# Optimization experiments

Hardware: AMD Instinct MI355X
Metric: run time of the kernel (lower is better)

Reference implementation:

```python
import jax, jax.numpy as jnp
import numpy as np

L, N = 200, 256  # event_list_length, num_nodes


def setup_inputs() -> dict:
    key = jax.random.key(0)
    ks = jax.random.split(key, 7)
    time = jax.random.uniform(ks[0], (2,), dtype=jnp.float32)
    event_list = jax.random.normal(ks[1], (L + 1, N, N), dtype=jnp.float32)
    u_begin = jax.random.uniform(ks[2], (N, N, 3), dtype=jnp.float32)
    # xavier-ish scales for params
    a = jax.random.normal(ks[3], (L, N, N, 3), dtype=jnp.float32) * 0.05
    w = jax.random.normal(ks[4], (L, N, 1, N), dtype=jnp.float32) * 0.05
    liner_w = jax.random.normal(ks[5], (N, 3), dtype=jnp.float32) * 0.5
    liner_b = jax.random.normal(ks[6], (N,), dtype=jnp.float32) * 0.1
    return {"time": time, "event_list": event_list, "u_begin": u_begin,
            "a": a, "w": w, "liner_w": liner_w, "liner_b": liner_b,
            "batch_size": 2}


def reference(time, event_list, u_begin, a, w, liner_w, liner_b, batch_size):
    # event_list[:-1]; consumed in pairs (start, start+1) with batch_size == 2
    T = event_list.shape[0] - 1
    S = T // batch_size                      # number of scan steps
    n = event_list.shape[1]
    e2 = event_list[:T].reshape(S, 2, n, n)          # [S,2,N,N]
    a2 = a[:T].reshape(S, 2, n, n, 3)                # [S,2,N,N,3]
    w2 = w[:T, :, 0, :].reshape(S, 2, n, n)          # [S,2,N,N] (squeeze the 1-dim)
    t0, t1 = time[0], time[1]                        # original always uses time[0], time[1]

    def step(u, xs):
        ep, ap, wp = xs                              # [2,N,N], [2,N,N,3], [2,N,N]
        # per-node scalar dot: w[start][node] @ event_begin[k][node]
        dot0 = jnp.einsum('nk,nk->n', wp[0], ep[0])  # [N]
        dot1 = jnp.einsum('nk,nk->n', wp[1], ep[1])
        # math.exp in the original returns a Python float -> constant w.r.t. autograd
        f0 = jax.lax.stop_gradient(jnp.exp(-dot0 * t0))[:, None, None]
        f1 = jax.lax.stop_gradient(jnp.exp(-dot1 * t1))[:, None, None]
        lamda = u + ap[0] * f0 + ap[1] * f1          # [N,N,3]
        temp = jax.nn.softmax(lamda, axis=-1)        # softmax over the 3-dim (dim=1 of [N,3] per node)
        # per-node Linear(3,1): temp[node] @ W_node^T + b_node -> [N,N]
        out = jnp.einsum('nmc,nc->nm', temp, liner_w) + liner_b[:, None]
        # state update was .detach().cpu().numpy() -> stop_gradient
        return jax.lax.stop_gradient(temp), out

    _, outs = jax.lax.scan(step, u_begin, (e2, a2, w2))
    return outs                                      # [S, N, N] == [T/2, N, N]
```

## Files before the change

kernel.cpp:

```cpp
#include <hip/hip_runtime.h>


#define NN 256
#define TT 200
#define SS 100
#define DEPTH 5

__global__ __launch_bounds__(256) void f_kernel(
    const float* __restrict__ timep,
    const float* __restrict__ ev,
    const float* __restrict__ w,
    float* __restrict__ fs)
{
    const int lane = threadIdx.x & 63;
    const int gwave = blockIdx.x * 4 + (threadIdx.x >> 6);
    const int t = gwave >> 8;
    const int n = gwave & 255;

    const size_t rowoff = (size_t)t * (NN * NN) + (size_t)n * NN;
    const float4* wp = (const float4*)(w + rowoff);
    const float4* ep = (const float4*)(ev + rowoff);
    float4 wv = wp[lane];
    float4 evv = ep[lane];
    float d = wv.x * evv.x;
    d = fmaf(wv.y, evv.y, d);
    d = fmaf(wv.z, evv.z, d);
    d = fmaf(wv.w, evv.w, d);
#pragma unroll
    for (int off = 1; off < 64; off <<= 1)
        d += __shfl_xor(d, off, 64);

    if (lane == 0) {
        const float tsel = (t & 1) ? timep[1] : timep[0];
        fs[n * TT + t] = __expf(-d * tsel);
    }
}

__global__ __launch_bounds__(256) void scan_kernel(
    const float* __restrict__ fs_g,
    const float* __restrict__ ub,
    const float* __restrict__ a,
    const float* __restrict__ lw,
    const float* __restrict__ lb,
    float* __restrict__ out)
{
    __shared__ float fs[TT];

    const int n = blockIdx.x;
    const int m = threadIdx.x;

    if (m < TT) fs[m] = fs_g[n * TT + m];
    __syncthreads();

    const size_t base    = (size_t)n * (NN * 3) + (size_t)m * 3;
    const size_t TSTRIDE = (size_t)NN * NN * 3;
    const float* ap = a + base;

    float u0 = ub[base + 0];
    float u1 = ub[base + 1];
    float u2 = ub[base + 2];

    const float w0 = lw[n * 3 + 0];
    const float w1 = lw[n * 3 + 1];
    const float w2 = lw[n * 3 + 2];
    const float bb = lb[n];

    float* op = out + (size_t)n * NN + m;

    float buf[DEPTH][6];
#pragma unroll
    for (int d = 0; d < DEPTH; ++d) {
        const float* app = ap + (size_t)(2 * d) * TSTRIDE;
        buf[d][0] = app[0];
        buf[d][1] = app[1];
        buf[d][2] = app[2];
        buf[d][3] = app[TSTRIDE + 0];
        buf[d][4] = app[TSTRIDE + 1];
        buf[d][5] = app[TSTRIDE + 2];
    }

    for (int s0 = 0; s0 < SS; s0 += DEPTH) {
#pragma unroll
        for (int d = 0; d < DEPTH; ++d) {
            const int s = s0 + d;

            const float f0 = fs[2 * s];
            const float f1 = fs[2 * s + 1];

            float l0 = fmaf(buf[d][0], f0, fmaf(buf[d][3], f1, u0));
            float l1 = fmaf(buf[d][1], f0, fmaf(buf[d][4], f1, u1));
            float l2 = fmaf(buf[d][2], f0, fmaf(buf[d][5], f1, u2));

            const int sp = (s + DEPTH < SS) ? (s + DEPTH) : 0;
            const float* app = ap + (size_t)(2 * sp) * TSTRIDE;
            buf[d][0] = app[0];
            buf[d][1] = app[1];
            buf[d][2] = app[2];
            buf[d][3] = app[TSTRIDE + 0];
            buf[d][4] = app[TSTRIDE + 1];
            buf[d][5] = app[TSTRIDE + 2];

            float mx = fmaxf(l0, fmaxf(l1, l2));
            float e0 = __expf(l0 - mx);
            float e1 = __expf(l1 - mx);
            float e2 = __expf(l2 - mx);
            float inv = __builtin_amdgcn_rcpf(e0 + e1 + e2);
            u0 = e0 * inv;
            u1 = e1 * inv;
            u2 = e2 * inv;
            op[(size_t)s * (NN * NN)] = fmaf(u0, w0, fmaf(u1, w1, fmaf(u2, w2, bb)));
        }
    }
}

extern "C" void kernel_launch(void* const* d_in, const int* in_sizes, int n_in,
                              void* d_out, int out_size, void* d_ws, size_t ws_size,
                              hipStream_t stream) {
    const float* timep = (const float*)d_in[0];
    const float* ev    = (const float*)d_in[1];
    const float* ub    = (const float*)d_in[2];
    const float* a     = (const float*)d_in[3];
    const float* w     = (const float*)d_in[4];
    const float* lw    = (const float*)d_in[5];
    const float* lb    = (const float*)d_in[6];
    float* out = (float*)d_out;
    float* fs  = (float*)d_ws;

    f_kernel<<<(TT * NN) / 4, 256, 0, stream>>>(timep, ev, w, fs);
    scan_kernel<<<NN, 256, 0, stream>>>(fs, ub, a, lw, lb, out);
}
```

Before: 305.7 us.

## Stage scan inputs through double-buffered LDS with async global loads and split rows

```diff
diff --git a/kernel.cpp b/kernel.cpp
--- a/kernel.cpp
+++ b/kernel.cpp
@@ -4,7 +4,15 @@
 #define NN 256
 #define TT 200
 #define SS 100
-#define DEPTH 5
+#define CH 10
+#define SLABS (2*CH)
+#define HALF 128
+#define SEG (HALF*3)
+#define CHUNKF (SLABS*SEG)
+#define NCHUNK (SS/CH)
+
+typedef const __attribute__((address_space(1))) void* gas1;
+typedef __attribute__((address_space(3))) void* las3;
 
 __global__ __launch_bounds__(256) void f_kernel(
     const float* __restrict__ timep,
@@ -12,31 +20,36 @@
     const float* __restrict__ w,
     float* __restrict__ fs)
 {
-    const int lane = threadIdx.x & 63;
+    const int lane  = threadIdx.x & 63;
     const int gwave = blockIdx.x * 4 + (threadIdx.x >> 6);
-    const int t = gwave >> 8;
-    const int n = gwave & 255;
+    const int n  = gwave & 255;
+    const int tp = gwave >> 8;
+    const int ta = 2 * tp;
 
-    const size_t rowoff = (size_t)t * (NN * NN) + (size_t)n * NN;
-    const float4* wp = (const float4*)(w + rowoff);
-    const float4* ep = (const float4*)(ev + rowoff);
-    float4 wv = wp[lane];
-    float4 evv = ep[lane];
-    float d = wv.x * evv.x;
-    d = fmaf(wv.y, evv.y, d);
-    d = fmaf(wv.z, evv.z, d);
-    d = fmaf(wv.w, evv.w, d);
+    const size_t ro_a = (size_t)ta * (NN * NN) + (size_t)n * NN;
+    const size_t ro_b = ro_a + (size_t)(NN * NN);
+    float4 wa = ((const float4*)(w  + ro_a))[lane];
+    float4 ea = ((const float4*)(ev + ro_a))[lane];
+    float4 wb = ((const float4*)(w  + ro_b))[lane];
+    float4 eb = ((const float4*)(ev + ro_b))[lane];
+    float da = wa.x * ea.x;
+    da = fmaf(wa.y, ea.y, da); da = fmaf(wa.z, ea.z, da); da = fmaf(wa.w, ea.w, da);
+    float db = wb.x * eb.x;
+    db = fmaf(wb.y, eb.y, db); db = fmaf(wb.z, eb.z, db); db = fmaf(wb.w, eb.w, db);
 #pragma unroll
-    for (int off = 1; off < 64; off <<= 1)
-        d += __shfl_xor(d, off, 64);
-
+    for (int off = 1; off < 64; off <<= 1) {
+        da += __shfl_xor(da, off, 64);
+        db += __shfl_xor(db, off, 64);
+    }
     if (lane == 0) {
-        const float tsel = (t & 1) ? timep[1] : timep[0];
-        fs[n * TT + t] = __expf(-d * tsel);
+        float2 r;
+        r.x = __expf(-da * timep[0]);
+        r.y = __expf(-db * timep[1]);
+        ((float2*)(fs + (size_t)n * TT))[tp] = r;
     }
 }
 
-__global__ __launch_bounds__(256) void scan_kernel(
+__global__ __launch_bounds__(HALF) void scan_kernel(
     const float* __restrict__ fs_g,
     const float* __restrict__ ub,
     const float* __restrict__ a,
@@ -45,71 +58,70 @@
     float* __restrict__ out)
 {
     __shared__ float fs[TT];
+    __shared__ float buf[2][CHUNKF];
 
-    const int n = blockIdx.x;
-    const int m = threadIdx.x;
+    const int nb   = blockIdx.x >> 1;
+    const int h    = blockIdx.x & 1;
+    const int mm   = threadIdx.x;
+    const int lane = mm & 63;
+    const int wid  = mm >> 6;
 
-    if (m < TT) fs[m] = fs_g[n * TT + m];
+    if (mm < TT) fs[mm] = fs_g[(size_t)nb * TT + mm];
+    if (mm + HALF < TT) fs[mm + HALF] = fs_g[(size_t)nb * TT + mm + HALF];
+
+    const size_t rowbase = (size_t)nb * 768 + (size_t)h * SEG;
+    const size_t TS = (size_t)NN * NN * 3;
+
+    auto fill = [&](int c, int which) {
+#pragma unroll
+        for (int r = 0; r < 15; ++r) {
+            const unsigned base4 = (unsigned)((r * 2 + wid) * 64);
+            const unsigned q  = base4 + (unsigned)lane;
+            const unsigned tl = q / 96;
+            const unsigned o4 = q - tl * 96;
+            const float* g = a + (size_t)(c * SLABS + tl) * TS + rowbase + (size_t)o4 * 4;
+            float* l = &buf[which][(size_t)base4 * 4];
+            __builtin_amdgcn_global_load_lds((gas1)g, (las3)l, 16, 0, 0);
+        }
+    };
+
+    fill(0, 0);
+
+    float u0, u1, u2;
+    {
+        const size_t b = rowbase + (size_t)mm * 3;
+        u0 = ub[b + 0]; u1 = ub[b + 1]; u2 = ub[b + 2];
+    }
+    const float w0 = lw[nb * 3 + 0];
+    const float w1 = lw[nb * 3 + 1];
+    const float w2 = lw[nb * 3 + 2];
+    const float bbias = lb[nb];
+    float* op = out + (size_t)nb * NN + (size_t)h * HALF + mm;
+
     __syncthreads();
 
-    const size_t base    = (size_t)n * (NN * 3) + (size_t)m * 3;
-    const size_t TSTRIDE = (size_t)NN * NN * 3;
-    const float* ap = a + base;
-
-    float u0 = ub[base + 0];
-    float u1 = ub[base + 1];
-    float u2 = ub[base + 2];
-
-    const float w0 = lw[n * 3 + 0];
-    const float w1 = lw[n * 3 + 1];
-    const float w2 = lw[n * 3 + 2];
-    const float bb = lb[n];
-
-    float* op = out + (size_t)n * NN + m;
-
-    float buf[DEPTH][6];
+    for (int c = 0; c < NCHUNK; ++c) {
+        if (c + 1 < NCHUNK) fill(c + 1, (c + 1) & 1);
+        const float* B = buf[c & 1];
 #pragma unroll
-    for (int d = 0; d < DEPTH; ++d) {
-        const float* app = ap + (size_t)(2 * d) * TSTRIDE;
-        buf[d][0] = app[0];
-        buf[d][1] = app[1];
-        buf[d][2] = app[2];
-        buf[d][3] = app[TSTRIDE + 0];
-        buf[d][4] = app[TSTRIDE + 1];
-        buf[d][5] = app[TSTRIDE + 2];
-    }
-
-    for (int s0 = 0; s0 < SS; s0 += DEPTH) {
-#pragma unroll
-        for (int d = 0; d < DEPTH; ++d) {
-            const int s = s0 + d;
-
+        for (int k = 0; k < CH; ++k) {
+            const int s = c * CH + k;
+            const float* s0 = B + (size_t)(2 * k) * SEG + (size_t)mm * 3;
+            const float* s1 = s0 + SEG;
             const float f0 = fs[2 * s];
             const float f1 = fs[2 * s + 1];
-
-            float l0 = fmaf(buf[d][0], f0, fmaf(buf[d][3], f1, u0));
-            float l1 = fmaf(buf[d][1], f0, fmaf(buf[d][4], f1, u1));
-            float l2 = fmaf(buf[d][2], f0, fmaf(buf[d][5], f1, u2));
-
-            const int sp = (s + DEPTH < SS) ? (s + DEPTH) : 0;
-            const float* app = ap + (size_t)(2 * sp) * TSTRIDE;
-            buf[d][0] = app[0];
-            buf[d][1] = app[1];
-            buf[d][2] = app[2];
-            buf[d][3] = app[TSTRIDE + 0];
-            buf[d][4] = app[TSTRIDE + 1];
-            buf[d][5] = app[TSTRIDE + 2];
-
+            float l0 = fmaf(s0[0], f0, fmaf(s1[0], f1, u0));
+            float l1 = fmaf(s0[1], f0, fmaf(s1[1], f1, u1));
+            float l2 = fmaf(s0[2], f0, fmaf(s1[2], f1, u2));
             float mx = fmaxf(l0, fmaxf(l1, l2));
             float e0 = __expf(l0 - mx);
             float e1 = __expf(l1 - mx);
             float e2 = __expf(l2 - mx);
             float inv = __builtin_amdgcn_rcpf(e0 + e1 + e2);
-            u0 = e0 * inv;
-            u1 = e1 * inv;
-            u2 = e2 * inv;
-            op[(size_t)s * (NN * NN)] = fmaf(u0, w0, fmaf(u1, w1, fmaf(u2, w2, bb)));
+            u0 = e0 * inv; u1 = e1 * inv; u2 = e2 * inv;
+            op[(size_t)s * (NN * NN)] = fmaf(u0, w0, fmaf(u1, w1, fmaf(u2, w2, bbias)));
         }
+        __syncthreads();
     }
 }
 
@@ -126,6 +138,6 @@
     float* out = (float*)d_out;
     float* fs  = (float*)d_ws;
 
-    f_kernel<<<(TT * NN) / 4, 256, 0, stream>>>(timep, ev, w, fs);
-    scan_kernel<<<NN, 256, 0, stream>>>(fs, ub, a, lw, lb, out);
+    f_kernel<<<(SS * NN) / 4, 256, 0, stream>>>(timep, ev, w, fs);
+    scan_kernel<<<2 * NN, HALF, 0, stream>>>(fs, ub, a, lw, lb, out);
 }
```

After: 309.3 us. Within noise of the previous version (+1.2%).
